# Optimization experiments

Hardware: AMD Instinct MI355X
Metric: run time of the kernel (lower is better)

## Reference

```python
import jax, jax.numpy as jnp
import numpy as np

N_NODES = 200000
IN_DIM = 128
HID = 64
WALK_LEN = 16          # max_step + 1
NUM_WALKS = 16         # = hidden_graphs, walks per graph
N_GRAPHS = 1024
PEN = 32
N_CLASSES = 10
BN_EPS = 1e-5


def setup_inputs() -> dict:
    key = jax.random.key(0)
    ks = jax.random.split(key, 16)
    x = jax.random.normal(ks[0], (N_NODES, IN_DIM), dtype=jnp.float32)
    walks = jax.random.randint(ks[1], (N_GRAPHS * NUM_WALKS, WALK_LEN), 0, N_NODES)
    # each graph contributes NUM_WALKS consecutive walks
    walk_batch = jnp.repeat(jnp.arange(N_GRAPHS), NUM_WALKS)
    s = 1.0 / np.sqrt(HID)
    return {
        "x": x,
        "walks": walks,
        "walk_batch": walk_batch,
        "W_enc": jax.random.normal(ks[2], (HID, IN_DIM), jnp.float32) / np.sqrt(IN_DIM),
        "b_enc": jnp.zeros((HID,), jnp.float32),
        "W_ih": jax.random.uniform(ks[3], (3 * HID, HID), jnp.float32, -s, s),
        "W_hh": jax.random.uniform(ks[4], (3 * HID, HID), jnp.float32, -s, s),
        "b_ih": jax.random.uniform(ks[5], (3 * HID,), jnp.float32, -s, s),
        "b_hh": jax.random.uniform(ks[6], (3 * HID,), jnp.float32, -s, s),
        "gamma": jnp.ones((HID,), jnp.float32),
        "beta": jnp.zeros((HID,), jnp.float32),
        "W1": jax.random.normal(ks[7], (PEN, HID), jnp.float32) / np.sqrt(HID),
        "b1": jnp.zeros((PEN,), jnp.float32),
        "W2": jax.random.normal(ks[8], (N_CLASSES, PEN), jnp.float32) / np.sqrt(PEN),
        "b2": jnp.zeros((N_CLASSES,), jnp.float32),
    }


def _gru_cell(h, xt, W_ih, W_hh, b_ih, b_hh):
    # PyTorch GRU gate math
    gi = xt @ W_ih.T + b_ih            # [W, 3H]
    gh = h @ W_hh.T + b_hh             # [W, 3H]
    i_r, i_z, i_n = jnp.split(gi, 3, axis=-1)
    h_r, h_z, h_n = jnp.split(gh, 3, axis=-1)
    r = jax.nn.sigmoid(i_r + h_r)
    z = jax.nn.sigmoid(i_z + h_z)
    n = jnp.tanh(i_n + r * h_n)
    return (1.0 - z) * n + z * h


def reference(x, walks, walk_batch, W_enc, b_enc, W_ih, W_hh, b_ih, b_hh,
              gamma, beta, W1, b1, W2, b2):
    # feature encoder on all nodes, then gather along walks
    x_enc = x @ W_enc.T + b_enc                     # [N, H]
    walk_feats = x_enc[walks]                       # [W, L, H] gather
    xs = jnp.swapaxes(walk_feats, 0, 1)             # [L, W, H]

    def step(h, xt):
        return _gru_cell(h, xt, W_ih, W_hh, b_ih, b_hh), None

    h0 = jnp.zeros((walks.shape[0], HID), walk_feats.dtype)
    h_final, _ = jax.lax.scan(step, h0, xs)         # [W, H] last hidden state

    # segment-mean pooling per graph
    seg_sum = jax.ops.segment_sum(h_final, walk_batch, num_segments=N_GRAPHS)
    cnt = jax.ops.segment_sum(jnp.ones((walks.shape[0],), h_final.dtype),
                              walk_batch, num_segments=N_GRAPHS)
    graph_enc = seg_sum / jnp.maximum(cnt, 1.0)[:, None]   # [B, H]

    # BatchNorm1d (training mode: batch statistics, biased variance)
    mean = jnp.mean(graph_enc, axis=0)
    var = jnp.mean(jnp.square(graph_enc - mean), axis=0)
    gn = (graph_enc - mean) / jnp.sqrt(var + BN_EPS) * gamma + beta

    h1 = jax.nn.relu(gn @ W1.T + b1)                # dropout p=0 -> identity
    logits = h1 @ W2.T + b2
    return jax.nn.log_softmax(logits, axis=1)
```

## Files before the change

### kernel.cpp

```cpp
#include <hip/hip_runtime.h>
#include <stdint.h>

typedef _Float16 half8 __attribute__((ext_vector_type(8)));
typedef _Float16 half4 __attribute__((ext_vector_type(4)));
typedef float f32x4 __attribute__((ext_vector_type(4)));

#define MFMA_F16(A, B, C) __builtin_amdgcn_mfma_f32_16x16x32_f16(A, B, C, 0, 0, 0)

#define NN 200000
#define NT 3125
#define GSTRIDE 512

__device__ __forceinline__ half8 cvt8(const float* p) {
  half8 a;
#pragma unroll
  for (int e = 0; e < 8; ++e) a[e] = (_Float16)p[e];
  return a;
}

__device__ __forceinline__ void gload_lds16(const void* gp, void* lp) {
  __builtin_amdgcn_global_load_lds(
      (const __attribute__((address_space(1))) uint32_t*)(gp),
      (__attribute__((address_space(3))) uint32_t*)(lp), 16, 0, 0);
}

__global__ __launch_bounds__(256, 2) void k_enc(const float* __restrict__ x,
                                                const float* __restrict__ Wenc,
                                                const float* __restrict__ benc,
                                                _Float16* __restrict__ xenc) {
  __shared__ float xl[2][64 * 128];
  __shared__ _Float16 wlds[16 * 64 * 8];

  const int tid = threadIdx.x;
  const int lane = tid & 63, wv = tid >> 6;
  const int r = lane & 15, g = lane >> 4;

  const int t0 = blockIdx.x;
#pragma unroll
  for (int i = 0; i < 8; ++i) {
    int row = wv * 16 + 2 * i + (lane >> 5);
    int grow = t0 * 64 + row;
    if (grow >= NN) grow = NN - 1;
    int scol = ((lane & 31) * 16) ^ ((row & 7) << 4);
    gload_lds16((const char*)(x + (size_t)grow * 128) + scol,
                (char*)&xl[0][0] + (wv * 16 + 2 * i) * 512);
  }

  for (int i4 = tid; i4 < 2048; i4 += 256) {
    int idx = i4 * 4;
    f32x4 v = *(const f32x4*)(Wenc + idx);
    int j = idx >> 7, k = idx & 127;
    int tile = (j >> 4) * 4 + (k >> 5);
    int ln = ((k >> 3) & 3) * 16 + (j & 15);
    half4 h;
    h[0] = (_Float16)v[0]; h[1] = (_Float16)v[1];
    h[2] = (_Float16)v[2]; h[3] = (_Float16)v[3];
    *(half4*)&wlds[(tile * 64 + ln) * 8 + (k & 7)] = h;
  }
  __syncthreads();

  half8 W[4][4];
#pragma unroll
  for (int jt = 0; jt < 4; ++jt)
#pragma unroll
    for (int kt = 0; kt < 4; ++kt)
      W[jt][kt] = *(const half8*)&wlds[((jt * 4 + kt) * 64 + lane) * 8];

  float bb[4][4];
#pragma unroll
  for (int jt = 0; jt < 4; ++jt)
#pragma unroll
    for (int rr = 0; rr < 4; ++rr) bb[jt][rr] = benc[jt * 16 + g * 4 + rr];

  const int sw = (r & 7) << 4;
  int buf = 0;

  for (int t = t0; t < NT; t += GSTRIDE) {
    int tn = t + GSTRIDE;
    if (tn < NT) {
#pragma unroll
      for (int i = 0; i < 8; ++i) {
        int row = wv * 16 + 2 * i + (lane >> 5);
        int grow = tn * 64 + row;
        if (grow >= NN) grow = NN - 1;
        int scol = ((lane & 31) * 16) ^ ((row & 7) << 4);
        gload_lds16((const char*)(x + (size_t)grow * 128) + scol,
                    (char*)&xl[buf ^ 1][0] + (wv * 16 + 2 * i) * 512);
      }
      asm volatile("s_waitcnt vmcnt(8)" ::: "memory");
    } else {
      asm volatile("s_waitcnt vmcnt(0)" ::: "memory");
    }
    __builtin_amdgcn_sched_barrier(0);

    const char* rp = (const char*)&xl[buf][0] + (wv * 16 + r) * 512;
    f32x4 acc[4];
#pragma unroll
    for (int jt = 0; jt < 4; ++jt)
      acc[jt] = (f32x4){bb[jt][0], bb[jt][1], bb[jt][2], bb[jt][3]};

#pragma unroll
    for (int kt = 0; kt < 4; ++kt) {
      f32x4 v0 = *(const f32x4*)(rp + ((kt * 128 + g * 32) ^ sw));
      f32x4 v1 = *(const f32x4*)(rp + ((kt * 128 + g * 32 + 16) ^ sw));
      half8 a;
#pragma unroll
      for (int e = 0; e < 4; ++e) {
        a[e] = (_Float16)v0[e];
        a[4 + e] = (_Float16)v1[e];
      }
#pragma unroll
      for (int jt = 0; jt < 4; ++jt)
        acc[jt] = MFMA_F16(W[jt][kt], a, acc[jt]);
    }

    int node = t * 64 + wv * 16 + r;
    if (node < NN) {
#pragma unroll
      for (int jt = 0; jt < 4; ++jt) {
        half4 o;
        o[0] = (_Float16)acc[jt][0]; o[1] = (_Float16)acc[jt][1];
        o[2] = (_Float16)acc[jt][2]; o[3] = (_Float16)acc[jt][3];
        *(half4*)&xenc[(size_t)node * 64 + jt * 16 + g * 4] = o;
      }
    }
    buf ^= 1;
  }
}

__global__ __launch_bounds__(256, 2) void k_gru(const _Float16* __restrict__ xenc,
                                                const int* __restrict__ walks,
                                                const float* __restrict__ Wih,
                                                const float* __restrict__ Whh,
                                                const float* __restrict__ bih,
                                                const float* __restrict__ bhh,
                                                float* __restrict__ genc) {
  __shared__ _Float16 wih_lds[24 * 64 * 8];
  __shared__ _Float16 whh_lds[24 * 64 * 8];
  __shared__ _Float16 h_lds[2][2][16 * 64];
  __shared__ int ids[2][256];

  const int tid = threadIdx.x;
  const int lane = tid & 63, wv = tid >> 6;
  const int r = lane & 15, g = lane >> 4;
  const int p = wv & 1;
  const int gl = wv >> 1;
  const int gph = blockIdx.x * 2 + gl;

  for (int idx = tid; idx < 192 * 64; idx += 256) {
    int j = idx >> 6, k = idx & 63;
    int tile = (j >> 4) * 2 + (k >> 5);
    int ln = ((k >> 3) & 3) * 16 + (j & 15);
    int off = (tile * 64 + ln) * 8 + (k & 7);
    wih_lds[off] = (_Float16)Wih[idx];
    whh_lds[off] = (_Float16)Whh[idx];
  }

  if (p == 0) {
    const int* wp = walks + gph * 256;
    int4 v = *(const int4*)(wp + lane * 4);
    int vals[4] = {v.x, v.y, v.z, v.w};
#pragma unroll
    for (int i = 0; i < 4; ++i) {
      int m = lane * 4 + i;
      ids[gl][(m & 15) * 16 + (m >> 4)] = vals[i];
    }
  }

  for (int i = tid; i < 2048; i += 256)
    ((_Float16*)h_lds)[(i >> 10) * 2048 + (i & 1023)] = (_Float16)0.f;

  __syncthreads();

  half8 Bi[3][2][2], Bh[3][2][2];
#pragma unroll
  for (int G = 0; G < 3; ++G)
#pragma unroll
    for (int jt = 0; jt < 2; ++jt)
#pragma unroll
      for (int kt = 0; kt < 2; ++kt) {
        int T = G * 4 + p * 2 + jt;
        Bi[G][jt][kt] = *(const half8*)&wih_lds[((T * 2 + kt) * 64 + lane) * 8];
        Bh[G][jt][kt] = *(const half8*)&whh_lds[((T * 2 + kt) * 64 + lane) * 8];
      }

  float br[2], bz[2], bin_[2], bhn_[2];
#pragma unroll
  for (int jt = 0; jt < 2; ++jt) {
    int j0 = (p * 2 + jt) * 16 + r;
    br[jt] = bih[j0] + bhh[j0];
    bz[jt] = bih[64 + j0] + bhh[64 + j0];
    bin_[jt] = bih[128 + j0];
    bhn_[jt] = bhh[128 + j0];
  }

  f32x4 h[2];
#pragma unroll
  for (int jt = 0; jt < 2; ++jt) h[jt] = (f32x4){0.f, 0.f, 0.f, 0.f};

  const int swz = (r & 7) << 4;

  half8 AxA0, AxA1, AxB0, AxB1;
  {
    int n0 = ids[gl][0 * 16 + r];
    const _Float16* p0 = xenc + (size_t)n0 * 64 + g * 8;
    AxA0 = *(const half8*)p0;
    AxA1 = *(const half8*)(p0 + 32);
    int n1 = ids[gl][1 * 16 + r];
    const _Float16* p1 = xenc + (size_t)n1 * 64 + g * 8;
    AxB0 = *(const half8*)p1;
    AxB1 = *(const half8*)(p1 + 32);
  }

#define GRU_STEP(T, RB, AX0, AX1)                                              \
  {                                                                            \
    char* rbase = (char*)&h_lds[gl][RB][0];                                    \
    char* wbase = (char*)&h_lds[gl][RB ^ 1][0];                                \
    half8 Ah0 = *(const half8*)(rbase + ((r * 128 + g * 16) ^ swz));           \
    half8 Ah1 = *(const half8*)(rbase + ((r * 128 + 64 + g * 16) ^ swz));      \
    f32x4 aR[2], aZ[2], aN[2], aH[2];                                          \
    _Pragma("unroll") for (int jt = 0; jt < 2; ++jt) {                         \
      aR[jt] = (f32x4){br[jt], br[jt], br[jt], br[jt]};                        \
      aZ[jt] = (f32x4){bz[jt], bz[jt], bz[jt], bz[jt]};                        \
      aN[jt] = (f32x4){bin_[jt], bin_[jt], bin_[jt], bin_[jt]};                \
      aH[jt] = (f32x4){bhn_[jt], bhn_[jt], bhn_[jt], bhn_[jt]};                \
    }                                                                          \
    _Pragma("unroll") for (int jt = 0; jt < 2; ++jt) {                         \
      aR[jt] = MFMA_F16(AX0, Bi[0][jt][0], aR[jt]);                            \
      aR[jt] = MFMA_F16(AX1, Bi[0][jt][1], aR[jt]);                            \
      aZ[jt] = MFMA_F16(AX0, Bi[1][jt][0], aZ[jt]);                            \
      aZ[jt] = MFMA_F16(AX1, Bi[1][jt][1], aZ[jt]);                            \
      aN[jt] = MFMA_F16(AX0, Bi[2][jt][0], aN[jt]);                            \
      aN[jt] = MFMA_F16(AX1, Bi[2][jt][1], aN[jt]);                            \
    }                                                                          \
    {                                                                          \
      int nid = ids[gl][(((T) + 2) & 15) * 16 + r];                            \
      const _Float16* xp = xenc + (size_t)nid * 64 + g * 8;                    \
      AX0 = *(const half8*)xp;                                                 \
      AX1 = *(const half8*)(xp + 32);                                          \
    }                                                                          \
    _Pragma("unroll") for (int jt = 0; jt < 2; ++jt) {                         \
      aR[jt] = MFMA_F16(Ah0, Bh[0][jt][0], aR[jt]);                            \
      aR[jt] = MFMA_F16(Ah1, Bh[0][jt][1], aR[jt]);                            \
      aZ[jt] = MFMA_F16(Ah0, Bh[1][jt][0], aZ[jt]);                            \
      aZ[jt] = MFMA_F16(Ah1, Bh[1][jt][1], aZ[jt]);                            \
      aH[jt] = MFMA_F16(Ah0, Bh[2][jt][0], aH[jt]);                            \
      aH[jt] = MFMA_F16(Ah1, Bh[2][jt][1], aH[jt]);                            \
    }                                                                          \
    _Pragma("unroll") for (int jt = 0; jt < 2; ++jt)                           \
        _Pragma("unroll") for (int rr = 0; rr < 4; ++rr) {                     \
      float pr = aR[jt][rr];                                                   \
      float pz = aZ[jt][rr];                                                   \
      float rg = __builtin_amdgcn_rcpf(1.f + __expf(-pr));                     \
      float zg = __builtin_amdgcn_rcpf(1.f + __expf(-pz));                     \
      float pn = aN[jt][rr] + rg * aH[jt][rr];                                 \
      float e2 = __expf(2.f * pn);                                             \
      float nn = 1.f - 2.f * __builtin_amdgcn_rcpf(e2 + 1.f);                  \
      h[jt][rr] = (1.f - zg) * nn + zg * h[jt][rr];                           \
    }                                                                          \
    if ((T) < 15) {                                                            \
      _Pragma("unroll") for (int jt = 0; jt < 2; ++jt)                         \
          _Pragma("unroll") for (int rr = 0; rr < 4; ++rr) {                   \
        int row = g * 4 + rr;                                                  \
        int jg = (p * 2 + jt) * 16 + r;                                        \
        int byte = (row * 128 + jg * 2) ^ ((row & 7) << 4);                    \
        *(_Float16*)(wbase + byte) = (_Float16)h[jt][rr];                      \
      }                                                                        \
    }                                                                          \
    __syncthreads();                                                           \
  }

  for (int t = 0; t < 16; t += 2) {
    GRU_STEP(t, 0, AxA0, AxA1);
    GRU_STEP(t + 1, 1, AxB0, AxB1);
  }
#undef GRU_STEP

#pragma unroll
  for (int jt = 0; jt < 2; ++jt) {
    float s = h[jt][0] + h[jt][1] + h[jt][2] + h[jt][3];
    s += __shfl_xor(s, 16);
    s += __shfl_xor(s, 32);
    if (g == 0) genc[gph * 64 + (p * 2 + jt) * 16 + r] = s * 0.0625f;
  }
}

__global__ __launch_bounds__(1024) void k_stats(const float* __restrict__ genc,
                                                const float* __restrict__ gamma,
                                                const float* __restrict__ beta,
                                                float* __restrict__ ss) {
  __shared__ float sum_s[16][64], sq_s[16][64];
  int j = threadIdx.x & 63, grp = threadIdx.x >> 6;
  float s = 0.f, q = 0.f;
#pragma unroll 4
  for (int rr = 0; rr < 64; ++rr) {
    float v = genc[(grp * 64 + rr) * 64 + j];
    s += v;
    q += v * v;
  }
  sum_s[grp][j] = s;
  sq_s[grp][j] = q;
  __syncthreads();
  if (grp == 0) {
    float S = 0.f, Q = 0.f;
#pragma unroll
    for (int k = 0; k < 16; ++k) {
      S += sum_s[k][j];
      Q += sq_s[k][j];
    }
    float mean = S * (1.f / 1024.f);
    float var = Q * (1.f / 1024.f) - mean * mean;
    float rstd = rsqrtf(var + 1e-5f);
    float sc = gamma[j] * rstd;
    ss[j] = sc;
    ss[64 + j] = beta[j] - mean * sc;
  }
}

__global__ __launch_bounds__(256, 1) void k_mlp(const float* __restrict__ genc,
                                                const float* __restrict__ ss,
                                                const float* __restrict__ W1,
                                                const float* __restrict__ b1,
                                                const float* __restrict__ W2,
                                                const float* __restrict__ b2,
                                                float* __restrict__ out) {
  __shared__ float w1[32 * 64], w2[10 * 32], bb1[32], bb2[10], sc[64], sh[64];
  const int tid = threadIdx.x;
  for (int i = tid; i < 32 * 64; i += 256) w1[i] = W1[i];
  for (int i = tid; i < 10 * 32; i += 256) w2[i] = W2[i];
  if (tid < 32) bb1[tid] = b1[tid];
  if (tid >= 32 && tid < 42) bb2[tid - 32] = b2[tid - 32];
  if (tid >= 64 && tid < 128) sc[tid - 64] = ss[tid - 64];
  if (tid >= 128 && tid < 192) sh[tid - 128] = ss[64 + tid - 128];
  __syncthreads();

  const int row = blockIdx.x * 256 + tid;
  float gn[64];
  const f32x4* gp = (const f32x4*)(genc + row * 64);
#pragma unroll
  for (int jq = 0; jq < 16; ++jq) {
    f32x4 v = gp[jq];
#pragma unroll
    for (int e = 0; e < 4; ++e) gn[jq * 4 + e] = v[e] * sc[jq * 4 + e] + sh[jq * 4 + e];
  }

  float h1[32];
#pragma unroll
  for (int i = 0; i < 32; ++i) {
    float a = bb1[i];
#pragma unroll
    for (int j = 0; j < 64; ++j) a += w1[i * 64 + j] * gn[j];
    h1[i] = fmaxf(a, 0.f);
  }

  float lg[10];
  float mx = -1e30f;
#pragma unroll
  for (int c = 0; c < 10; ++c) {
    float a = bb2[c];
#pragma unroll
    for (int i = 0; i < 32; ++i) a += w2[c * 32 + i] * h1[i];
    lg[c] = a;
    mx = fmaxf(mx, a);
  }
  float se = 0.f;
#pragma unroll
  for (int c = 0; c < 10; ++c) se += __expf(lg[c] - mx);
  float lse = mx + __logf(se);
#pragma unroll
  for (int c = 0; c < 10; ++c) out[row * 10 + c] = lg[c] - lse;
}

extern "C" void kernel_launch(void* const* d_in, const int* in_sizes, int n_in,
                              void* d_out, int out_size, void* d_ws, size_t ws_size,
                              hipStream_t stream) {
  const float* x = (const float*)d_in[0];
  const int* walks = (const int*)d_in[1];
  const float* Wenc = (const float*)d_in[3];
  const float* benc = (const float*)d_in[4];
  const float* Wih = (const float*)d_in[5];
  const float* Whh = (const float*)d_in[6];
  const float* bih = (const float*)d_in[7];
  const float* bhh = (const float*)d_in[8];
  const float* gamma = (const float*)d_in[9];
  const float* beta = (const float*)d_in[10];
  const float* W1 = (const float*)d_in[11];
  const float* b1 = (const float*)d_in[12];
  const float* W2 = (const float*)d_in[13];
  const float* b2 = (const float*)d_in[14];
  float* out = (float*)d_out;

  char* ws = (char*)d_ws;
  _Float16* xenc = (_Float16*)ws;
  float* genc = (float*)(ws + 25600000);
  float* ss = (float*)(ws + 25600000 + 262144);

  k_enc<<<dim3(GSTRIDE), dim3(256), 0, stream>>>(x, Wenc, benc, xenc);
  k_gru<<<dim3(512), dim3(256), 0, stream>>>(xenc, walks, Wih, Whh, bih, bhh, genc);
  k_stats<<<dim3(1), dim3(1024), 0, stream>>>(genc, gamma, beta, ss);
  k_mlp<<<dim3(4), dim3(256), 0, stream>>>(genc, ss, W1, b1, W2, b2, out);
}
```

Before: 84.04 us.

## Split GRU hidden columns across four waves per graph and lighten step barrier

The GRU kernel now runs 512 threads per block, with four waves per graph. Each wave owns one 16-column slice of the hidden state instead of two, which halves per-wave MFMA work and register use on the serial recurrence. The next-step gather is issued at the top of each step, and __syncthreads is replaced with an explicit lgkmcnt wait, s_barrier and sched_barrier. This trades more waves and more barrier participants for shorter per-step critical paths and better latency hiding.

```diff
diff --git a/kernel.cpp b/kernel.cpp
--- a/kernel.cpp
+++ b/kernel.cpp
@@ -10,13 +10,6 @@
 #define NN 200000
 #define NT 3125
 #define GSTRIDE 512
-
-__device__ __forceinline__ half8 cvt8(const float* p) {
-  half8 a;
-#pragma unroll
-  for (int e = 0; e < 8; ++e) a[e] = (_Float16)p[e];
-  return a;
-}
 
 __device__ __forceinline__ void gload_lds16(const void* gp, void* lp) {
   __builtin_amdgcn_global_load_lds(
@@ -128,7 +121,7 @@
   }
 }
 
-__global__ __launch_bounds__(256, 2) void k_gru(const _Float16* __restrict__ xenc,
+__global__ __launch_bounds__(512, 4) void k_gru(const _Float16* __restrict__ xenc,
                                                 const int* __restrict__ walks,
                                                 const float* __restrict__ Wih,
                                                 const float* __restrict__ Whh,
@@ -143,11 +136,11 @@
   const int tid = threadIdx.x;
   const int lane = tid & 63, wv = tid >> 6;
   const int r = lane & 15, g = lane >> 4;
-  const int p = wv & 1;
-  const int gl = wv >> 1;
+  const int p = wv & 3;
+  const int gl = wv >> 2;
   const int gph = blockIdx.x * 2 + gl;
 
-  for (int idx = tid; idx < 192 * 64; idx += 256) {
+  for (int idx = tid; idx < 192 * 64; idx += 512) {
     int j = idx >> 6, k = idx & 63;
     int tile = (j >> 4) * 2 + (k >> 5);
     int ln = ((k >> 3) & 3) * 16 + (j & 15);
@@ -156,7 +149,7 @@
     whh_lds[off] = (_Float16)Whh[idx];
   }
 
-  if (p == 0) {
+  if ((wv & 3) == 0) {
     const int* wp = walks + gph * 256;
     int4 v = *(const int4*)(wp + lane * 4);
     int vals[4] = {v.x, v.y, v.z, v.w};
@@ -167,37 +160,27 @@
     }
   }
 
-  for (int i = tid; i < 2048; i += 256)
-    ((_Float16*)h_lds)[(i >> 10) * 2048 + (i & 1023)] = (_Float16)0.f;
+  for (int i = tid; i < 4096; i += 512) ((_Float16*)h_lds)[i] = (_Float16)0.f;
 
   __syncthreads();
 
-  half8 Bi[3][2][2], Bh[3][2][2];
+  half8 Bi[3][2], Bh[3][2];
 #pragma unroll
   for (int G = 0; G < 3; ++G)
 #pragma unroll
-    for (int jt = 0; jt < 2; ++jt)
-#pragma unroll
-      for (int kt = 0; kt < 2; ++kt) {
-        int T = G * 4 + p * 2 + jt;
-        Bi[G][jt][kt] = *(const half8*)&wih_lds[((T * 2 + kt) * 64 + lane) * 8];
-        Bh[G][jt][kt] = *(const half8*)&whh_lds[((T * 2 + kt) * 64 + lane) * 8];
-      }
-
-  float br[2], bz[2], bin_[2], bhn_[2];
-#pragma unroll
-  for (int jt = 0; jt < 2; ++jt) {
-    int j0 = (p * 2 + jt) * 16 + r;
-    br[jt] = bih[j0] + bhh[j0];
-    bz[jt] = bih[64 + j0] + bhh[64 + j0];
-    bin_[jt] = bih[128 + j0];
-    bhn_[jt] = bhh[128 + j0];
-  }
-
-  f32x4 h[2];
-#pragma unroll
-  for (int jt = 0; jt < 2; ++jt) h[jt] = (f32x4){0.f, 0.f, 0.f, 0.f};
-
+    for (int kt = 0; kt < 2; ++kt) {
+      int T = G * 4 + p;
+      Bi[G][kt] = *(const half8*)&wih_lds[((T * 2 + kt) * 64 + lane) * 8];
+      Bh[G][kt] = *(const half8*)&whh_lds[((T * 2 + kt) * 64 + lane) * 8];
+    }
+
+  const int j0 = p * 16 + r;
+  const float br_ = bih[j0] + bhh[j0];
+  const float bz_ = bih[64 + j0] + bhh[64 + j0];
+  const float bin_ = bih[128 + j0];
+  const float bhn_ = bhh[128 + j0];
+
+  f32x4 h = (f32x4){0.f, 0.f, 0.f, 0.f};
   const int swz = (r & 7) << 4;
 
   half8 AxA0, AxA1, AxB0, AxB1;
@@ -212,62 +195,53 @@
     AxB1 = *(const half8*)(p1 + 32);
   }
 
-#define GRU_STEP(T, RB, AX0, AX1)                                              \
+#define GRU_STEP(T_, RB, AX0, AX1)                                             \
   {                                                                            \
+              \
+    int nid = ids[gl][(((T_) + 2) & 15) * 16 + r];                             \
+    const _Float16* xp = xenc + (size_t)nid * 64 + g * 8;                      \
+    half8 NX0 = *(const half8*)xp;                                             \
+    half8 NX1 = *(const half8*)(xp + 32);                                      \
     char* rbase = (char*)&h_lds[gl][RB][0];                                    \
     char* wbase = (char*)&h_lds[gl][RB ^ 1][0];                                \
     half8 Ah0 = *(const half8*)(rbase + ((r * 128 + g * 16) ^ swz));           \
     half8 Ah1 = *(const half8*)(rbase + ((r * 128 + 64 + g * 16) ^ swz));      \
-    f32x4 aR[2], aZ[2], aN[2], aH[2];                                          \
-    _Pragma("unroll") for (int jt = 0; jt < 2; ++jt) {                         \
-      aR[jt] = (f32x4){br[jt], br[jt], br[jt], br[jt]};                        \
-      aZ[jt] = (f32x4){bz[jt], bz[jt], bz[jt], bz[jt]};                        \
-      aN[jt] = (f32x4){bin_[jt], bin_[jt], bin_[jt], bin_[jt]};                \
-      aH[jt] = (f32x4){bhn_[jt], bhn_[jt], bhn_[jt], bhn_[jt]};                \
-    }                                                                          \
-    _Pragma("unroll") for (int jt = 0; jt < 2; ++jt) {                         \
-      aR[jt] = MFMA_F16(AX0, Bi[0][jt][0], aR[jt]);                            \
-      aR[jt] = MFMA_F16(AX1, Bi[0][jt][1], aR[jt]);                            \
-      aZ[jt] = MFMA_F16(AX0, Bi[1][jt][0], aZ[jt]);                            \
-      aZ[jt] = MFMA_F16(AX1, Bi[1][jt][1], aZ[jt]);                            \
-      aN[jt] = MFMA_F16(AX0, Bi[2][jt][0], aN[jt]);                            \
-      aN[jt] = MFMA_F16(AX1, Bi[2][jt][1], aN[jt]);                            \
-    }                                                                          \
-    {                                                                          \
-      int nid = ids[gl][(((T) + 2) & 15) * 16 + r];                            \
-      const _Float16* xp = xenc + (size_t)nid * 64 + g * 8;                    \
-      AX0 = *(const half8*)xp;                                                 \
-      AX1 = *(const half8*)(xp + 32);                                          \
-    }                                                                          \
-    _Pragma("unroll") for (int jt = 0; jt < 2; ++jt) {                         \
-      aR[jt] = MFMA_F16(Ah0, Bh[0][jt][0], aR[jt]);                            \
-      aR[jt] = MFMA_F16(Ah1, Bh[0][jt][1], aR[jt]);                            \
-      aZ[jt] = MFMA_F16(Ah0, Bh[1][jt][0], aZ[jt]);                            \
-      aZ[jt] = MFMA_F16(Ah1, Bh[1][jt][1], aZ[jt]);                            \
-      aH[jt] = MFMA_F16(Ah0, Bh[2][jt][0], aH[jt]);                            \
-      aH[jt] = MFMA_F16(Ah1, Bh[2][jt][1], aH[jt]);                            \
-    }                                                                          \
-    _Pragma("unroll") for (int jt = 0; jt < 2; ++jt)                           \
-        _Pragma("unroll") for (int rr = 0; rr < 4; ++rr) {                     \
-      float pr = aR[jt][rr];                                                   \
-      float pz = aZ[jt][rr];                                                   \
-      float rg = __builtin_amdgcn_rcpf(1.f + __expf(-pr));                     \
-      float zg = __builtin_amdgcn_rcpf(1.f + __expf(-pz));                     \
-      float pn = aN[jt][rr] + rg * aH[jt][rr];                                 \
+    f32x4 aR = (f32x4){br_, br_, br_, br_};                                    \
+    f32x4 aZ = (f32x4){bz_, bz_, bz_, bz_};                                    \
+    f32x4 aN = (f32x4){bin_, bin_, bin_, bin_};                                \
+    f32x4 aH = (f32x4){bhn_, bhn_, bhn_, bhn_};                                \
+    aR = MFMA_F16(AX0, Bi[0][0], aR);                                          \
+    aR = MFMA_F16(AX1, Bi[0][1], aR);                                          \
+    aZ = MFMA_F16(AX0, Bi[1][0], aZ);                                          \
+    aZ = MFMA_F16(AX1, Bi[1][1], aZ);                                          \
+    aN = MFMA_F16(AX0, Bi[2][0], aN);                                          \
+    aN = MFMA_F16(AX1, Bi[2][1], aN);                                          \
+    aR = MFMA_F16(Ah0, Bh[0][0], aR);                                          \
+    aR = MFMA_F16(Ah1, Bh[0][1], aR);                                          \
+    aZ = MFMA_F16(Ah0, Bh[1][0], aZ);                                          \
+    aZ = MFMA_F16(Ah1, Bh[1][1], aZ);                                          \
+    aH = MFMA_F16(Ah0, Bh[2][0], aH);                                          \
+    aH = MFMA_F16(Ah1, Bh[2][1], aH);                                          \
+    _Pragma("unroll") for (int rr = 0; rr < 4; ++rr) {                         \
+      float rg = __builtin_amdgcn_rcpf(1.f + __expf(-aR[rr]));                 \
+      float zg = __builtin_amdgcn_rcpf(1.f + __expf(-aZ[rr]));                 \
+      float pn = aN[rr] + rg * aH[rr];                                         \
       float e2 = __expf(2.f * pn);                                             \
       float nn = 1.f - 2.f * __builtin_amdgcn_rcpf(e2 + 1.f);                  \
-      h[jt][rr] = (1.f - zg) * nn + zg * h[jt][rr];                           \
+      h[rr] = (1.f - zg) * nn + zg * h[rr];                                    \
     }                                                                          \
-    if ((T) < 15) {                                                            \
-      _Pragma("unroll") for (int jt = 0; jt < 2; ++jt)                         \
-          _Pragma("unroll") for (int rr = 0; rr < 4; ++rr) {                   \
+    if ((T_) < 15) {                                                           \
+      _Pragma("unroll") for (int rr = 0; rr < 4; ++rr) {                       \
         int row = g * 4 + rr;                                                  \
-        int jg = (p * 2 + jt) * 16 + r;                                        \
-        int byte = (row * 128 + jg * 2) ^ ((row & 7) << 4);                    \
-        *(_Float16*)(wbase + byte) = (_Float16)h[jt][rr];                      \
+        int byte = (row * 128 + j0 * 2) ^ ((row & 7) << 4);                    \
+        *(_Float16*)(wbase + byte) = (_Float16)h[rr];                          \
       }                                                                        \
     }                                                                          \
-    __syncthreads();                                                           \
+    asm volatile("s_waitcnt lgkmcnt(0)" ::: "memory");                         \
+    __builtin_amdgcn_s_barrier();                                              \
+    __builtin_amdgcn_sched_barrier(0);                                         \
+    AX0 = NX0;                                                                 \
+    AX1 = NX1;                                                                 \
   }
 
   for (int t = 0; t < 16; t += 2) {
@@ -276,12 +250,11 @@
   }
 #undef GRU_STEP
 
-#pragma unroll
-  for (int jt = 0; jt < 2; ++jt) {
-    float s = h[jt][0] + h[jt][1] + h[jt][2] + h[jt][3];
+  {
+    float s = h[0] + h[1] + h[2] + h[3];
     s += __shfl_xor(s, 16);
     s += __shfl_xor(s, 32);
-    if (g == 0) genc[gph * 64 + (p * 2 + jt) * 16 + r] = s * 0.0625f;
+    if (g == 0) genc[gph * 64 + j0] = s * 0.0625f;
   }
 }
 
@@ -396,7 +369,7 @@
   float* ss = (float*)(ws + 25600000 + 262144);
 
   k_enc<<<dim3(GSTRIDE), dim3(256), 0, stream>>>(x, Wenc, benc, xenc);
-  k_gru<<<dim3(512), dim3(256), 0, stream>>>(xenc, walks, Wih, Whh, bih, bhh, genc);
+  k_gru<<<dim3(512), dim3(512), 0, stream>>>(xenc, walks, Wih, Whh, bih, bhh, genc);
   k_stats<<<dim3(1), dim3(1024), 0, stream>>>(genc, gamma, beta, ss);
   k_mlp<<<dim3(4), dim3(256), 0, stream>>>(genc, ss, W1, b1, W2, b2, out);
 }
```

Measured after the change: 82.19 us. 2.2% less time.
